# Optimization experiments

Measured on AMD Instinct MI355X. Metric: run time of the kernel, lower is better.

The kernel has to match this reference:

```python
import jax, jax.numpy as jnp
import numpy as np

NA = 100000  # number of a-type nodes (rows of adj)
NB = 100000  # number of b-type nodes (cols of adj)
NE = 1600000 # number of edges (nnz of adj)
BF = 128     # b_features
AF = 128     # a_features


def setup_inputs() -> dict:
    key = jax.random.key(0)
    k1, k2, k3, k4, k5, k6 = jax.random.split(key, 6)
    stdv = 1.0 / np.sqrt(BF)
    return {
        "b_input": jax.random.normal(k1, (NB, BF), dtype=jnp.float32),
        "edge_rows": jax.random.randint(k2, (NE,), 0, NA, dtype=jnp.int32),
        "edge_cols": jax.random.randint(k3, (NE,), 0, NB, dtype=jnp.int32),
        "edge_vals": jax.random.uniform(k4, (NE,), dtype=jnp.float32),
        "a_weight": jax.random.uniform(k5, (BF, AF), minval=-stdv, maxval=stdv, dtype=jnp.float32),
        "a_bias": jax.random.uniform(k6, (AF,), minval=-stdv, maxval=stdv, dtype=jnp.float32),
    }


def reference(b_input, edge_rows, edge_cols, edge_vals, a_weight, a_bias):
    # a_support = b_input @ a_weight            : [NB, AF]
    a_support = jnp.matmul(b_input, a_weight)
    # a_output = spmm(adj, a_support)           : [NA, AF]
    # adj[r, c] = edge_vals at (edge_rows, edge_cols)
    gathered = a_support[edge_cols] * edge_vals[:, None]   # [NE, AF]
    a_output = jax.ops.segment_sum(gathered, edge_rows, num_segments=NA)
    # bias=True -> early return of a-side output
    return a_output + a_bias
```

## Files before the change

### kernel.cpp

```cpp
#include <hip/hip_runtime.h>
#include <hip/hip_bf16.h>

#define AF 128
#define BF 128
#define BROWS 64
#define CAP_F 1600
#define SORT_CAP 1664
#define CROWS 1024
#define CAP_C 18432
#define CHUNK1 2048
#define NCOARSE_MAX 128

typedef __attribute__((ext_vector_type(8))) short bf16x8;
typedef __attribute__((ext_vector_type(4))) float f32x4;

__device__ inline unsigned short f2bf(float f) {
    unsigned int u = __float_as_uint(f);
    u += 0x7FFF + ((u >> 16) & 1);
    return (unsigned short)(u >> 16);
}
__device__ inline unsigned int pk2bf(float x, float y) {
    __hip_bfloat162 h = __float22bfloat162_rn(make_float2(x, y));
    return *(unsigned int*)&h;
}
__device__ inline float bflo(unsigned int u) { return __uint_as_float(u << 16); }
__device__ inline float bfhi(unsigned int u) { return __uint_as_float(u & 0xFFFF0000u); }

__global__ __launch_bounds__(256) void phase1_kernel(const float* __restrict__ Bin,
                                                     const float* __restrict__ W,
                                                     unsigned int* __restrict__ Sup, int NB,
                                                     const int* __restrict__ rows,
                                                     const int* __restrict__ cols,
                                                     const float* __restrict__ vals,
                                                     int* __restrict__ grelC,
                                                     int2* __restrict__ binnedC,
                                                     int NE, int NCOARSE, int ngemm) {
    __shared__ unsigned short Ws[128][136];
    __shared__ int h[NCOARSE_MAX];
    __shared__ int rbase[NCOARSE_MAX];
    const int tid = threadIdx.x;

    if ((int)blockIdx.x < ngemm) {
        const int lane = tid & 63;
        const int wave = tid >> 6;
        const int row0 = blockIdx.x * 64;
        const int m = lane & 15;
        const int quad = lane >> 4;

        {
            int k = tid >> 1;
            int n0 = (tid & 1) * 64;
            const float4* src = (const float4*)(W + (size_t)k * AF + n0);
            #pragma unroll
            for (int i = 0; i < 16; i++) {
                float4 v = src[i];
                int n = n0 + i * 4;
                Ws[n + 0][k] = f2bf(v.x);
                Ws[n + 1][k] = f2bf(v.y);
                Ws[n + 2][k] = f2bf(v.z);
                Ws[n + 3][k] = f2bf(v.w);
            }
        }
        int arow = row0 + wave * 16 + m;
        int arow_c = (arow < NB) ? arow : (NB - 1);
        const float* ap = Bin + (size_t)arow_c * BF + quad * 8;
        bf16x8 af[4];
        #pragma unroll
        for (int ks = 0; ks < 4; ks++) {
            float4 lo = *(const float4*)(ap + ks * 32);
            float4 hi = *(const float4*)(ap + ks * 32 + 4);
            union { unsigned int u[4]; bf16x8 v; } cv;
            cv.u[0] = pk2bf(lo.x, lo.y); cv.u[1] = pk2bf(lo.z, lo.w);
            cv.u[2] = pk2bf(hi.x, hi.y); cv.u[3] = pk2bf(hi.z, hi.w);
            af[ks] = cv.v;
        }
        __syncthreads();

        f32x4 acc[8];
        #pragma unroll
        for (int nt = 0; nt < 8; nt++) {
            f32x4 a = {0.f, 0.f, 0.f, 0.f};
            #pragma unroll
            for (int ks = 0; ks < 4; ks++) {
                bf16x8 bf = *(const bf16x8*)(&Ws[nt * 16 + m][ks * 32 + quad * 8]);
                a = __builtin_amdgcn_mfma_f32_16x16x32_bf16(af[ks], bf, a, 0, 0, 0);
            }
            acc[nt] = a;
        }
        #pragma unroll
        for (int nt = 0; nt < 4; nt++) {
            #pragma unroll
            for (int r = 0; r < 4; r++) {
                int row = row0 + wave * 16 + quad * 4 + r;
                if (row < NB)
                    Sup[(size_t)row * 64 + nt * 16 + m] = pk2bf(acc[nt][r], acc[nt + 4][r]);
            }
        }
    } else {
        int bid = blockIdx.x - ngemm;
        int base = bid * CHUNK1;
        int ke[8]; int px[8]; float pv[8];
        #pragma unroll
        for (int i = 0; i < 8; i++) {
            int e = base + tid + i * 256;
            if (e < NE) {
                int r = rows[e];
                ke[i] = r >> 10;
                px[i] = cols[e] | ((r & 1023) << 17);
                pv[i] = vals[e];
            } else ke[i] = -1;
        }
        if (tid < NCOARSE) h[tid] = 0;
        __syncthreads();
        #pragma unroll
        for (int i = 0; i < 8; i++)
            if (ke[i] >= 0) atomicAdd(&h[ke[i]], 1);
        __syncthreads();
        if (tid < NCOARSE) {
            int c = h[tid];
            rbase[tid] = tid * CAP_C + (c ? atomicAdd(&grelC[tid], c) : 0);
            h[tid] = 0;
        }
        __syncthreads();
        #pragma unroll
        for (int i = 0; i < 8; i++) {
            if (ke[i] >= 0) {
                int lp = atomicAdd(&h[ke[i]], 1);
                binnedC[rbase[ke[i]] + lp] = make_int2(px[i], __float_as_int(pv[i]));
            }
        }
    }
}

__global__ __launch_bounds__(256) void passA2_kernel(const int2* __restrict__ binnedC,
                                                     const int* __restrict__ grelC,
                                                     int* __restrict__ grelF,
                                                     int2* __restrict__ binnedF, int NBUCK) {
    __shared__ int h[16];
    __shared__ int rb[16];
    const int tid = threadIdx.x;
    const int j = blockIdx.x >> 4;
    const int s = blockIdx.x & 15;
    int n = grelC[j]; if (n > CAP_C) n = CAP_C;
    const int st = (n * s) >> 4;
    const int en = (n * (s + 1)) >> 4;
    const int2* src = binnedC + (size_t)j * CAP_C;

    int sub[5]; int qx[5]; int qy[5];
    #pragma unroll
    for (int i = 0; i < 5; i++) {
        int idx = st + tid + i * 256;
        if (idx < en) {
            int2 p = src[idx];
            sub[i] = p.x >> 23;
            qx[i] = p.x & 0x7FFFFF;
            qy[i] = p.y;
        } else sub[i] = -1;
    }
    if (tid < 16) h[tid] = 0;
    __syncthreads();
    #pragma unroll
    for (int i = 0; i < 5; i++)
        if (sub[i] >= 0) atomicAdd(&h[sub[i]], 1);
    __syncthreads();
    if (tid < 16) {
        int c = h[tid];
        int fine = j * 16 + tid;
        rb[tid] = (fine < NBUCK) ? (fine * CAP_F + (c ? atomicAdd(&grelF[fine], c) : 0)) : 0;
        h[tid] = 0;
    }
    __syncthreads();
    #pragma unroll
    for (int i = 0; i < 5; i++) {
        if (sub[i] >= 0) {
            int lp = atomicAdd(&h[sub[i]], 1);
            binnedF[(size_t)rb[sub[i]] + lp] = make_int2(qx[i], qy[i]);
        }
    }
}

__global__ __launch_bounds__(256) void spmm_sorted_kernel(const unsigned short* __restrict__ Sup,
                                                          const int2* __restrict__ binned,
                                                          const int* __restrict__ grel,
                                                          const float* __restrict__ bias,
                                                          float* __restrict__ out, int NA) {
    __shared__ int2 spxy[SORT_CAP];
    __shared__ int cnt[BROWS];
    __shared__ int rs[BROWS + 1];
    __shared__ int cur[BROWS];
    const int tid = threadIdx.x;
    const int b = blockIdx.x;
    int n = grel[b]; if (n > CAP_F) n = CAP_F;
    const int2* src = binned + (size_t)b * CAP_F;

    int2 pr[7];
    #pragma unroll
    for (int j = 0; j < 7; j++) {
        int i = tid + j * 256;
        pr[j] = (i < n) ? src[i] : make_int2(-1, 0);
    }
    if (tid < BROWS) cnt[tid] = 0;
    __syncthreads();
    #pragma unroll
    for (int j = 0; j < 7; j++)
        if (pr[j].x >= 0) atomicAdd(&cnt[(pr[j].x >> 17) & 63], 1);
    __syncthreads();
    if (tid < 64) {
        int v = (cnt[tid] + 7) & ~7;
        int x = v;
        #pragma unroll
        for (int off = 1; off < 64; off <<= 1) {
            int t = __shfl_up(x, off);
            if (tid >= off) x += t;
        }
        rs[tid] = x - v;
        cur[tid] = x - v;
        if (tid == 63) rs[64] = x;
    }
    __syncthreads();
    #pragma unroll
    for (int j = 0; j < 7; j++) {
        if (pr[j].x >= 0) {
            int lr = (pr[j].x >> 17) & 63;
            int pos = atomicAdd(&cur[lr], 1);
            spxy[pos] = make_int2(pr[j].x & 0x1FFFF, pr[j].y);
        }
    }
    __syncthreads();
    if (tid < BROWS) {
        int end = rs[tid + 1];
        for (int p = cur[tid]; p < end; p++) spxy[p] = make_int2(0, 0);
    }
    __syncthreads();

    const int lane = tid & 63;
    const int wv = tid >> 6;
    const float b0 = bias[lane];
    const float b1 = bias[64 + lane];
    for (int lr = wv; lr < BROWS; lr += 4) {
        int row = b * BROWS + lr;
        if (row >= NA) break;
        int e = rs[lr], end = rs[lr + 1];
        float ax = 0.f, ay = 0.f;
        for (; e < end; e += 8) {
            int2 q0 = spxy[e],     q1 = spxy[e + 1], q2 = spxy[e + 2], q3 = spxy[e + 3];
            int2 q4 = spxy[e + 4], q5 = spxy[e + 5], q6 = spxy[e + 6], q7 = spxy[e + 7];
            unsigned int s0 = *(const unsigned int*)(Sup + (size_t)q0.x * AF + lane * 2);
            unsigned int s1 = *(const unsigned int*)(Sup + (size_t)q1.x * AF + lane * 2);
            unsigned int s2 = *(const unsigned int*)(Sup + (size_t)q2.x * AF + lane * 2);
            unsigned int s3 = *(const unsigned int*)(Sup + (size_t)q3.x * AF + lane * 2);
            unsigned int s4 = *(const unsigned int*)(Sup + (size_t)q4.x * AF + lane * 2);
            unsigned int s5 = *(const unsigned int*)(Sup + (size_t)q5.x * AF + lane * 2);
            unsigned int s6 = *(const unsigned int*)(Sup + (size_t)q6.x * AF + lane * 2);
            unsigned int s7 = *(const unsigned int*)(Sup + (size_t)q7.x * AF + lane * 2);
            float v0 = __int_as_float(q0.y), v1 = __int_as_float(q1.y);
            float v2 = __int_as_float(q2.y), v3 = __int_as_float(q3.y);
            float v4 = __int_as_float(q4.y), v5 = __int_as_float(q5.y);
            float v6 = __int_as_float(q6.y), v7 = __int_as_float(q7.y);
            ax += v0 * bflo(s0) + v1 * bflo(s1) + v2 * bflo(s2) + v3 * bflo(s3)
                + v4 * bflo(s4) + v5 * bflo(s5) + v6 * bflo(s6) + v7 * bflo(s7);
            ay += v0 * bfhi(s0) + v1 * bfhi(s1) + v2 * bfhi(s2) + v3 * bfhi(s3)
                + v4 * bfhi(s4) + v5 * bfhi(s5) + v6 * bfhi(s6) + v7 * bfhi(s7);
        }
        out[(size_t)row * AF + lane]      = ax + b0;
        out[(size_t)row * AF + 64 + lane] = ay + b1;
    }
}

extern "C" void kernel_launch(void* const* d_in, const int* in_sizes, int n_in,
                              void* d_out, int out_size, void* d_ws, size_t ws_size,
                              hipStream_t stream) {
    const float* b_input   = (const float*)d_in[0];
    const int*   edge_rows = (const int*)d_in[1];
    const int*   edge_cols = (const int*)d_in[2];
    const float* edge_vals = (const float*)d_in[3];
    const float* a_weight  = (const float*)d_in[4];
    const float* a_bias    = (const float*)d_in[5];
    const int NB = in_sizes[0] / BF;
    const int NE = in_sizes[1];
    const int NA = out_size / AF;
    const int NBUCK = (NA + BROWS - 1) / BROWS;
    const int NCOARSE = (NA + CROWS - 1) / CROWS;
    float* out = (float*)d_out;

    char* ws = (char*)d_ws;
    size_t off = 0;
    unsigned short* Sup = (unsigned short*)(ws + off); off += (size_t)NB * AF * sizeof(unsigned short);
    int* grelC = (int*)(ws + off); off += 1024 * sizeof(int);
    int* grelF = (int*)(ws + off); off += 2048 * sizeof(int);
    int2* binnedC = (int2*)(ws + off); off += (size_t)NCOARSE * CAP_C * sizeof(int2);
    int2* binnedF = (int2*)(ws + off); off += (size_t)NBUCK * CAP_F * sizeof(int2);
    (void)ws_size; (void)n_in;

    hipMemsetAsync(grelC, 0, 3072 * sizeof(int), stream);

    const int ngemm = (NB + 63) / 64;
    const int npass = (NE + CHUNK1 - 1) / CHUNK1;
    phase1_kernel<<<ngemm + npass, 256, 0, stream>>>(
        b_input, a_weight, (unsigned int*)Sup, NB,
        edge_rows, edge_cols, edge_vals, grelC, binnedC, NE, NCOARSE, ngemm);
    passA2_kernel<<<NCOARSE * 16, 256, 0, stream>>>(binnedC, grelC, grelF, binnedF, NBUCK);
    spmm_sorted_kernel<<<NBUCK, 256, 0, stream>>>(Sup, binnedF, grelF, a_bias, out, NA);
}
```

Measured before the change: 222.9 us.

## Fuse fine binning into SpMM kernel, filtering coarse bins per block

Removes the separate fine-binning pass and its intermediate buffer. Each SpMM block now scans its whole coarse bin, keeps the edges belonging to its own 64-row sub-bucket using ballot compaction, then sorts them by row in shared memory. The block-to-bin mapping is interleaved so the 16 blocks sharing a coarse bin can hit it in cache. The gather loop is also restructured so each wave walks a contiguous 16-row range with 16-wide batches. The cost is that every coarse bin is read 16 times, and sub-buckets holding more than 1344 edges are silently truncated.

Measured after the change: 225.5 us. Within noise of the previous version (+1.2%).

```diff
diff --git a/kernel.cpp b/kernel.cpp
--- a/kernel.cpp
+++ b/kernel.cpp
@@ -4,10 +4,10 @@
 #define AF 128
 #define BF 128
 #define BROWS 64
-#define CAP_F 1600
-#define SORT_CAP 1664
 #define CROWS 1024
 #define CAP_C 18432
+#define MAXF 1344
+#define SORT_CAP 2304
 #define CHUNK1 2048
 #define NCOARSE_MAX 128
 
@@ -132,138 +132,147 @@
     }
 }
 
-__global__ __launch_bounds__(256) void passA2_kernel(const int2* __restrict__ binnedC,
-                                                     const int* __restrict__ grelC,
-                                                     int* __restrict__ grelF,
-                                                     int2* __restrict__ binnedF, int NBUCK) {
-    __shared__ int h[16];
-    __shared__ int rb[16];
-    const int tid = threadIdx.x;
-    const int j = blockIdx.x >> 4;
-    const int s = blockIdx.x & 15;
-    int n = grelC[j]; if (n > CAP_C) n = CAP_C;
-    const int st = (n * s) >> 4;
-    const int en = (n * (s + 1)) >> 4;
-    const int2* src = binnedC + (size_t)j * CAP_C;
-
-    int sub[5]; int qx[5]; int qy[5];
-    #pragma unroll
-    for (int i = 0; i < 5; i++) {
-        int idx = st + tid + i * 256;
-        if (idx < en) {
-            int2 p = src[idx];
-            sub[i] = p.x >> 23;
-            qx[i] = p.x & 0x7FFFFF;
-            qy[i] = p.y;
-        } else sub[i] = -1;
-    }
-    if (tid < 16) h[tid] = 0;
-    __syncthreads();
-    #pragma unroll
-    for (int i = 0; i < 5; i++)
-        if (sub[i] >= 0) atomicAdd(&h[sub[i]], 1);
-    __syncthreads();
-    if (tid < 16) {
-        int c = h[tid];
-        int fine = j * 16 + tid;
-        rb[tid] = (fine < NBUCK) ? (fine * CAP_F + (c ? atomicAdd(&grelF[fine], c) : 0)) : 0;
-        h[tid] = 0;
-    }
-    __syncthreads();
-    #pragma unroll
-    for (int i = 0; i < 5; i++) {
-        if (sub[i] >= 0) {
-            int lp = atomicAdd(&h[sub[i]], 1);
-            binnedF[(size_t)rb[sub[i]] + lp] = make_int2(qx[i], qy[i]);
-        }
-    }
-}
-
-__global__ __launch_bounds__(256) void spmm_sorted_kernel(const unsigned short* __restrict__ Sup,
-                                                          const int2* __restrict__ binned,
-                                                          const int* __restrict__ grel,
-                                                          const float* __restrict__ bias,
-                                                          float* __restrict__ out, int NA) {
-    __shared__ int2 spxy[SORT_CAP];
+__global__ __launch_bounds__(256) void spmm_fused_kernel(const unsigned short* __restrict__ Sup,
+                                                         const int2* __restrict__ binnedC,
+                                                         const int* __restrict__ grelC,
+                                                         const float* __restrict__ bias,
+                                                         float* __restrict__ out,
+                                                         int NA, int NBUCK, int NCOARSE) {
+    __shared__ int2 buf[SORT_CAP];
     __shared__ int cnt[BROWS];
     __shared__ int rs[BROWS + 1];
     __shared__ int cur[BROWS];
+    __shared__ int nstage;
     const int tid = threadIdx.x;
-    const int b = blockIdx.x;
-    int n = grel[b]; if (n > CAP_F) n = CAP_F;
-    const int2* src = binned + (size_t)b * CAP_F;
-
-    int2 pr[7];
+    const int lane = tid & 63;
+
+    const int hb = (int)blockIdx.x;
+    const int x = hb & 7;
+    const int k = hb >> 3;
+    const int jj = x + 8 * (k >> 4);
+    const int ss = k & 15;
+    const int fb = jj * 16 + ss;
+    if (jj >= NCOARSE || fb >= NBUCK) return;
+
+    int n = grelC[jj]; if (n > CAP_C) n = CAP_C;
+    const int4* src4 = (const int4*)(binnedC + (size_t)jj * CAP_C);
+
+    if (tid == 0) nstage = 0;
+    if (tid < BROWS) cnt[tid] = 0;
+    __syncthreads();
+
+    const int nPairs = (n + 1) >> 1;
+    const int iters = (nPairs + 255) >> 8;
+    for (int it = 0; it < iters; ++it) {
+        int i = (it << 8) + tid;
+        bool in = i < nPairs;
+        int4 p = src4[in ? i : 0];
+        bool k0 = in && (((p.x >> 23) & 15) == ss);
+        bool k1 = in && ((2 * i + 1) < n) && (((p.z >> 23) & 15) == ss);
+        unsigned long long m0 = __ballot(k0);
+        unsigned long long m1 = __ballot(k1);
+        int c0 = __popcll(m0);
+        int tot = c0 + __popcll(m1);
+        if (tot) {
+            int base = 0;
+            if (lane == 0) base = atomicAdd(&nstage, tot);
+            base = __shfl(base, 0);
+            unsigned long long below = (1ull << lane) - 1;
+            if (k0) {
+                int p0 = base + __popcll(m0 & below);
+                if (p0 < MAXF) buf[p0] = make_int2(p.x, p.y);
+            }
+            if (k1) {
+                int p1 = base + c0 + __popcll(m1 & below);
+                if (p1 < MAXF) buf[p1] = make_int2(p.z, p.w);
+            }
+        }
+    }
+    __syncthreads();
+
+    int total = nstage; if (total > MAXF) total = MAXF;
+
+    int2 pr[6];
     #pragma unroll
-    for (int j = 0; j < 7; j++) {
-        int i = tid + j * 256;
-        pr[j] = (i < n) ? src[i] : make_int2(-1, 0);
-    }
-    if (tid < BROWS) cnt[tid] = 0;
-    __syncthreads();
+    for (int q = 0; q < 6; q++) {
+        int i = tid + q * 256;
+        pr[q] = (i < total) ? buf[i] : make_int2(-1, 0);
+    }
     #pragma unroll
-    for (int j = 0; j < 7; j++)
-        if (pr[j].x >= 0) atomicAdd(&cnt[(pr[j].x >> 17) & 63], 1);
-    __syncthreads();
+    for (int q = 0; q < 6; q++)
+        if (pr[q].x >= 0) atomicAdd(&cnt[(pr[q].x >> 17) & 63], 1);
+    __syncthreads();
+
     if (tid < 64) {
-        int v = (cnt[tid] + 7) & ~7;
-        int x = v;
+        int v = (cnt[tid] + 15) & ~15;
+        int xp = v;
         #pragma unroll
         for (int off = 1; off < 64; off <<= 1) {
-            int t = __shfl_up(x, off);
-            if (tid >= off) x += t;
-        }
-        rs[tid] = x - v;
-        cur[tid] = x - v;
-        if (tid == 63) rs[64] = x;
-    }
-    __syncthreads();
+            int t = __shfl_up(xp, off);
+            if (tid >= off) xp += t;
+        }
+        rs[tid] = xp - v;
+        cur[tid] = xp - v;
+        if (tid == 63) rs[64] = xp;
+    }
+    __syncthreads();
+
     #pragma unroll
-    for (int j = 0; j < 7; j++) {
-        if (pr[j].x >= 0) {
-            int lr = (pr[j].x >> 17) & 63;
+    for (int q = 0; q < 6; q++) {
+        if (pr[q].x >= 0) {
+            int lr = (pr[q].x >> 17) & 63;
             int pos = atomicAdd(&cur[lr], 1);
-            spxy[pos] = make_int2(pr[j].x & 0x1FFFF, pr[j].y);
+            buf[pos] = make_int2(pr[q].x & 0x1FFFF, pr[q].y);
         }
     }
     __syncthreads();
     if (tid < BROWS) {
         int end = rs[tid + 1];
-        for (int p = cur[tid]; p < end; p++) spxy[p] = make_int2(0, 0);
-    }
-    __syncthreads();
-
-    const int lane = tid & 63;
+        for (int p = cur[tid]; p < end; p++) buf[p] = make_int2(0, 0);
+    }
+    __syncthreads();
+
     const int wv = tid >> 6;
     const float b0 = bias[lane];
     const float b1 = bias[64 + lane];
-    for (int lr = wv; lr < BROWS; lr += 4) {
-        int row = b * BROWS + lr;
-        if (row >= NA) break;
-        int e = rs[lr], end = rs[lr + 1];
-        float ax = 0.f, ay = 0.f;
-        for (; e < end; e += 8) {
-            int2 q0 = spxy[e],     q1 = spxy[e + 1], q2 = spxy[e + 2], q3 = spxy[e + 3];
-            int2 q4 = spxy[e + 4], q5 = spxy[e + 5], q6 = spxy[e + 6], q7 = spxy[e + 7];
-            unsigned int s0 = *(const unsigned int*)(Sup + (size_t)q0.x * AF + lane * 2);
-            unsigned int s1 = *(const unsigned int*)(Sup + (size_t)q1.x * AF + lane * 2);
-            unsigned int s2 = *(const unsigned int*)(Sup + (size_t)q2.x * AF + lane * 2);
-            unsigned int s3 = *(const unsigned int*)(Sup + (size_t)q3.x * AF + lane * 2);
-            unsigned int s4 = *(const unsigned int*)(Sup + (size_t)q4.x * AF + lane * 2);
-            unsigned int s5 = *(const unsigned int*)(Sup + (size_t)q5.x * AF + lane * 2);
-            unsigned int s6 = *(const unsigned int*)(Sup + (size_t)q6.x * AF + lane * 2);
-            unsigned int s7 = *(const unsigned int*)(Sup + (size_t)q7.x * AF + lane * 2);
-            float v0 = __int_as_float(q0.y), v1 = __int_as_float(q1.y);
-            float v2 = __int_as_float(q2.y), v3 = __int_as_float(q3.y);
-            float v4 = __int_as_float(q4.y), v5 = __int_as_float(q5.y);
-            float v6 = __int_as_float(q6.y), v7 = __int_as_float(q7.y);
-            ax += v0 * bflo(s0) + v1 * bflo(s1) + v2 * bflo(s2) + v3 * bflo(s3)
-                + v4 * bflo(s4) + v5 * bflo(s5) + v6 * bflo(s6) + v7 * bflo(s7);
-            ay += v0 * bfhi(s0) + v1 * bfhi(s1) + v2 * bfhi(s2) + v3 * bfhi(s3)
-                + v4 * bfhi(s4) + v5 * bfhi(s5) + v6 * bfhi(s6) + v7 * bfhi(s7);
-        }
-        out[(size_t)row * AF + lane]      = ax + b0;
-        out[(size_t)row * AF + 64 + lane] = ay + b1;
+    int r = wv * 16;
+    const int rend = r + 16;
+    int e = rs[r];
+    const int eend = rs[rend];
+    int nb = rs[r + 1];
+    float ax = 0.f, ay = 0.f;
+    for (; e < eend; e += 16) {
+        while (e >= nb) {
+            int row = fb * BROWS + r;
+            if (row < NA) {
+                out[(size_t)row * AF + lane]      = ax + b0;
+                out[(size_t)row * AF + 64 + lane] = ay + b1;
+            }
+            ax = 0.f; ay = 0.f;
+            ++r; nb = rs[r + 1];
+        }
+        int2 q[16];
+        #pragma unroll
+        for (int t = 0; t < 16; t++) q[t] = buf[e + t];
+        unsigned int su[16];
+        #pragma unroll
+        for (int t = 0; t < 16; t++)
+            su[t] = *(const unsigned int*)(Sup + (size_t)q[t].x * AF + lane * 2);
+        #pragma unroll
+        for (int t = 0; t < 16; t++) {
+            float v = __int_as_float(q[t].y);
+            ax += v * bflo(su[t]);
+            ay += v * bfhi(su[t]);
+        }
+    }
+    while (r < rend) {
+        int row = fb * BROWS + r;
+        if (row < NA) {
+            out[(size_t)row * AF + lane]      = ax + b0;
+            out[(size_t)row * AF + 64 + lane] = ay + b1;
+        }
+        ax = 0.f; ay = 0.f;
+        ++r;
     }
 }
 
@@ -287,18 +296,18 @@
     size_t off = 0;
     unsigned short* Sup = (unsigned short*)(ws + off); off += (size_t)NB * AF * sizeof(unsigned short);
     int* grelC = (int*)(ws + off); off += 1024 * sizeof(int);
-    int* grelF = (int*)(ws + off); off += 2048 * sizeof(int);
     int2* binnedC = (int2*)(ws + off); off += (size_t)NCOARSE * CAP_C * sizeof(int2);
-    int2* binnedF = (int2*)(ws + off); off += (size_t)NBUCK * CAP_F * sizeof(int2);
     (void)ws_size; (void)n_in;
 
-    hipMemsetAsync(grelC, 0, 3072 * sizeof(int), stream);
+    hipMemsetAsync(grelC, 0, 1024 * sizeof(int), stream);
 
     const int ngemm = (NB + 63) / 64;
     const int npass = (NE + CHUNK1 - 1) / CHUNK1;
     phase1_kernel<<<ngemm + npass, 256, 0, stream>>>(
         b_input, a_weight, (unsigned int*)Sup, NB,
         edge_rows, edge_cols, edge_vals, grelC, binnedC, NE, NCOARSE, ngemm);
-    passA2_kernel<<<NCOARSE * 16, 256, 0, stream>>>(binnedC, grelC, grelF, binnedF, NBUCK);
-    spmm_sorted_kernel<<<NBUCK, 256, 0, stream>>>(Sup, binnedF, grelF, a_bias, out, NA);
-}
+
+    const int nco8 = (NCOARSE + 7) & ~7;
+    spmm_fused_kernel<<<nco8 * 16, 256, 0, stream>>>(
+        Sup, binnedC, grelC, a_bias, out, NA, NBUCK, NCOARSE);
+}
```

## Pretranspose weights in a prep kernel and software-pipeline SpMM gathers across rows

Applied to the files above, without the earlier changes.

A small prep kernel converts the weight matrix to a transposed bf16 copy once and zeroes the histogram counters, replacing the memset and removing the per-block LDS transpose and barrier from every GEMM block. The GEMM blocks now read B fragments directly from global memory or cache. The SpMM kernel now gives each wave a contiguous span of 16 rows and walks their edges as one stream, prefetching the next 8 gathered rows while accumulating the current ones, so short rows no longer stall on load latency. SORT_CAP grows, which may raise LDS use and cost occupancy.

New measurement: 226.1 us. About the same (+1.4%).

```diff
diff --git a/kernel.cpp b/kernel.cpp
--- a/kernel.cpp
+++ b/kernel.cpp
@@ -5,7 +5,7 @@
 #define BF 128
 #define BROWS 64
 #define CAP_F 1600
-#define SORT_CAP 1664
+#define SORT_CAP 2048
 #define CROWS 1024
 #define CAP_C 18432
 #define CHUNK1 2048
@@ -26,8 +26,23 @@
 __device__ inline float bflo(unsigned int u) { return __uint_as_float(u << 16); }
 __device__ inline float bfhi(unsigned int u) { return __uint_as_float(u & 0xFFFF0000u); }
 
+__global__ __launch_bounds__(256) void prep_kernel(const float* __restrict__ W,
+                                                   unsigned short* __restrict__ Wt,
+                                                   int* __restrict__ grelC,
+                                                   int* __restrict__ grelF) {
+    const int idx = blockIdx.x * 256 + threadIdx.x;
+    const int n = idx >> 7, k = idx & 127;
+    Wt[idx] = f2bf(W[(size_t)k * AF + n]);
+    if (blockIdx.x == 0) {
+        #pragma unroll
+        for (int i = threadIdx.x; i < 1024; i += 256) grelC[i] = 0;
+        #pragma unroll
+        for (int i = threadIdx.x; i < 2048; i += 256) grelF[i] = 0;
+    }
+}
+
 __global__ __launch_bounds__(256) void phase1_kernel(const float* __restrict__ Bin,
-                                                     const float* __restrict__ W,
+                                                     const unsigned short* __restrict__ Wt,
                                                      unsigned int* __restrict__ Sup, int NB,
                                                      const int* __restrict__ rows,
                                                      const int* __restrict__ cols,
@@ -35,7 +50,6 @@
                                                      int* __restrict__ grelC,
                                                      int2* __restrict__ binnedC,
                                                      int NE, int NCOARSE, int ngemm) {
-    __shared__ unsigned short Ws[128][136];
     __shared__ int h[NCOARSE_MAX];
     __shared__ int rbase[NCOARSE_MAX];
     const int tid = threadIdx.x;
@@ -47,20 +61,6 @@
         const int m = lane & 15;
         const int quad = lane >> 4;
 
-        {
-            int k = tid >> 1;
-            int n0 = (tid & 1) * 64;
-            const float4* src = (const float4*)(W + (size_t)k * AF + n0);
-            #pragma unroll
-            for (int i = 0; i < 16; i++) {
-                float4 v = src[i];
-                int n = n0 + i * 4;
-                Ws[n + 0][k] = f2bf(v.x);
-                Ws[n + 1][k] = f2bf(v.y);
-                Ws[n + 2][k] = f2bf(v.z);
-                Ws[n + 3][k] = f2bf(v.w);
-            }
-        }
         int arow = row0 + wave * 16 + m;
         int arow_c = (arow < NB) ? arow : (NB - 1);
         const float* ap = Bin + (size_t)arow_c * BF + quad * 8;
@@ -74,15 +74,15 @@
             cv.u[2] = pk2bf(hi.x, hi.y); cv.u[3] = pk2bf(hi.z, hi.w);
             af[ks] = cv.v;
         }
-        __syncthreads();
 
         f32x4 acc[8];
         #pragma unroll
         for (int nt = 0; nt < 8; nt++) {
             f32x4 a = {0.f, 0.f, 0.f, 0.f};
+            const unsigned short* wp = Wt + (size_t)(nt * 16 + m) * 128 + quad * 8;
             #pragma unroll
             for (int ks = 0; ks < 4; ks++) {
-                bf16x8 bf = *(const bf16x8*)(&Ws[nt * 16 + m][ks * 32 + quad * 8]);
+                bf16x8 bf = *(const bf16x8*)(wp + ks * 32);
                 a = __builtin_amdgcn_mfma_f32_16x16x32_bf16(af[ks], bf, a, 0, 0, 0);
             }
             acc[nt] = a;
@@ -237,33 +237,58 @@
     const int wv = tid >> 6;
     const float b0 = bias[lane];
     const float b1 = bias[64 + lane];
-    for (int lr = wv; lr < BROWS; lr += 4) {
-        int row = b * BROWS + lr;
-        if (row >= NA) break;
-        int e = rs[lr], end = rs[lr + 1];
-        float ax = 0.f, ay = 0.f;
-        for (; e < end; e += 8) {
-            int2 q0 = spxy[e],     q1 = spxy[e + 1], q2 = spxy[e + 2], q3 = spxy[e + 3];
-            int2 q4 = spxy[e + 4], q5 = spxy[e + 5], q6 = spxy[e + 6], q7 = spxy[e + 7];
-            unsigned int s0 = *(const unsigned int*)(Sup + (size_t)q0.x * AF + lane * 2);
-            unsigned int s1 = *(const unsigned int*)(Sup + (size_t)q1.x * AF + lane * 2);
-            unsigned int s2 = *(const unsigned int*)(Sup + (size_t)q2.x * AF + lane * 2);
-            unsigned int s3 = *(const unsigned int*)(Sup + (size_t)q3.x * AF + lane * 2);
-            unsigned int s4 = *(const unsigned int*)(Sup + (size_t)q4.x * AF + lane * 2);
-            unsigned int s5 = *(const unsigned int*)(Sup + (size_t)q5.x * AF + lane * 2);
-            unsigned int s6 = *(const unsigned int*)(Sup + (size_t)q6.x * AF + lane * 2);
-            unsigned int s7 = *(const unsigned int*)(Sup + (size_t)q7.x * AF + lane * 2);
-            float v0 = __int_as_float(q0.y), v1 = __int_as_float(q1.y);
-            float v2 = __int_as_float(q2.y), v3 = __int_as_float(q3.y);
-            float v4 = __int_as_float(q4.y), v5 = __int_as_float(q5.y);
-            float v6 = __int_as_float(q6.y), v7 = __int_as_float(q7.y);
-            ax += v0 * bflo(s0) + v1 * bflo(s1) + v2 * bflo(s2) + v3 * bflo(s3)
-                + v4 * bflo(s4) + v5 * bflo(s5) + v6 * bflo(s6) + v7 * bflo(s7);
-            ay += v0 * bfhi(s0) + v1 * bfhi(s1) + v2 * bfhi(s2) + v3 * bfhi(s3)
-                + v4 * bfhi(s4) + v5 * bfhi(s5) + v6 * bfhi(s6) + v7 * bfhi(s7);
-        }
-        out[(size_t)row * AF + lane]      = ax + b0;
-        out[(size_t)row * AF + 64 + lane] = ay + b1;
+    int r = wv * 16;
+    const int rend = r + 16;
+    int e = rs[r];
+    const int eend = rs[rend];
+    int nb = rs[r + 1];
+    float ax = 0.f, ay = 0.f;
+
+    int2 q[8]; unsigned int su[8];
+    if (e < eend) {
+        #pragma unroll
+        for (int t = 0; t < 8; t++) q[t] = spxy[e + t];
+        #pragma unroll
+        for (int t = 0; t < 8; t++)
+            su[t] = *(const unsigned int*)(Sup + (size_t)q[t].x * AF + lane * 2);
+    }
+    while (e < eend) {
+        const int en2 = e + 8;
+        int2 q2[8]; unsigned int s2[8];
+        if (en2 < eend) {
+            #pragma unroll
+            for (int t = 0; t < 8; t++) q2[t] = spxy[en2 + t];
+            #pragma unroll
+            for (int t = 0; t < 8; t++)
+                s2[t] = *(const unsigned int*)(Sup + (size_t)q2[t].x * AF + lane * 2);
+        }
+        while (e >= nb) {
+            int row = b * BROWS + r;
+            if (row < NA) {
+                out[(size_t)row * AF + lane]      = ax + b0;
+                out[(size_t)row * AF + 64 + lane] = ay + b1;
+            }
+            ax = 0.f; ay = 0.f;
+            ++r; nb = rs[r + 1];
+        }
+        #pragma unroll
+        for (int t = 0; t < 8; t++) {
+            float v = __int_as_float(q[t].y);
+            ax += v * bflo(su[t]);
+            ay += v * bfhi(su[t]);
+        }
+        #pragma unroll
+        for (int t = 0; t < 8; t++) { q[t] = q2[t]; su[t] = s2[t]; }
+        e = en2;
+    }
+    while (r < rend) {
+        int row = b * BROWS + r;
+        if (row < NA) {
+            out[(size_t)row * AF + lane]      = ax + b0;
+            out[(size_t)row * AF + 64 + lane] = ay + b1;
+        }
+        ax = 0.f; ay = 0.f;
+        ++r;
     }
 }
 
@@ -288,16 +313,16 @@
     unsigned short* Sup = (unsigned short*)(ws + off); off += (size_t)NB * AF * sizeof(unsigned short);
     int* grelC = (int*)(ws + off); off += 1024 * sizeof(int);
     int* grelF = (int*)(ws + off); off += 2048 * sizeof(int);
+    unsigned short* Wt = (unsigned short*)(ws + off); off += (size_t)128 * 128 * sizeof(unsigned short);
     int2* binnedC = (int2*)(ws + off); off += (size_t)NCOARSE * CAP_C * sizeof(int2);
     int2* binnedF = (int2*)(ws + off); off += (size_t)NBUCK * CAP_F * sizeof(int2);
     (void)ws_size; (void)n_in;
 
-    hipMemsetAsync(grelC, 0, 3072 * sizeof(int), stream);
-
     const int ngemm = (NB + 63) / 64;
     const int npass = (NE + CHUNK1 - 1) / CHUNK1;
+    prep_kernel<<<64, 256, 0, stream>>>(a_weight, Wt, grelC, grelF);
     phase1_kernel<<<ngemm + npass, 256, 0, stream>>>(
-        b_input, a_weight, (unsigned int*)Sup, NB,
+        b_input, Wt, (unsigned int*)Sup, NB,
         edge_rows, edge_cols, edge_vals, grelC, binnedC, NE, NCOARSE, ngemm);
     passA2_kernel<<<NCOARSE * 16, 256, 0, stream>>>(binnedC, grelC, grelF, binnedF, NBUCK);
     spmm_sorted_kernel<<<NBUCK, 256, 0, stream>>>(Sup, binnedF, grelF, a_bias, out, NA);
```
